# Kernel tuning notes

Measured on AMD Instinct MI355X. Metric: run time of the kernel, lower is better.

The kernel has to match this reference:

```python
import jax, jax.numpy as jnp
import numpy as np

N = 50000       # nodes
D_IN = 256      # in_channels
D_OUT = 256     # out_channels
E1 = 300000     # edges for TAGConv branch
E2 = 300000     # edges for attention branch


def setup_inputs() -> dict:
    key = jax.random.key(0)
    ks = jax.random.split(key, 8)
    s = 1.0 / np.sqrt(D_IN)  # torch Linear default init range
    u = lambda k: jax.random.uniform(k, (D_IN, D_OUT), jnp.float32, -s, s)
    return {
        "x": jax.random.normal(ks[0], (N, D_IN), jnp.float32),
        "edge_index": jax.random.randint(ks[1], (2, E1), 0, N),
        "edge_index_2": jax.random.randint(ks[2], (2, E2), 0, N),
        "W0": u(ks[3]),  # TAGConv hop-0 weight
        "W1": u(ks[4]),  # TAGConv hop-1 weight
        "Wq": u(ks[5]),  # attention query proj
        "Wk": u(ks[6]),  # attention key proj
        "Wv": u(ks[7]),  # attention value proj
    }


def reference(x, edge_index, edge_index_2, W0, W1, Wq, Wk, Wv):
    # --- TAGConv branch: K=1, normalize=False, bias=False ---
    src, dst = edge_index[0], edge_index[1]
    agg = jax.ops.segment_sum(x[src], dst, num_segments=N)   # A @ x, [N, D_IN]
    x1 = x @ W0 + agg @ W1                                   # [N, D_OUT]

    # --- Transformer_Block branch over edge_index_2, use_softmax=False ---
    q = x @ Wq
    k = x @ Wk
    v = x @ Wv
    s2, d2 = edge_index_2[0], edge_index_2[1]
    attn = jnp.einsum('ed,ed->e', q[d2], k[s2])              # per-edge raw score
    x2 = jax.ops.segment_sum(attn[:, None] * v[s2], d2, num_segments=N)

    return x1 - x2
```

## Files before the change

kernel.cpp:

```cpp
#include <hip/hip_runtime.h>

#define TD 256

typedef __attribute__((ext_vector_type(8))) short short8;
typedef __attribute__((ext_vector_type(8))) unsigned short ushort8;
typedef __attribute__((ext_vector_type(4))) float f32x4;

__device__ inline unsigned short f2bf(float f) {
  unsigned u = __float_as_uint(f);
  u = u + 0x7fffu + ((u >> 16) & 1u);
  return (unsigned short)(u >> 16);
}
__device__ inline float bf2f(unsigned short h) {
  return __uint_as_float(((unsigned)h) << 16);
}

__global__ __launch_bounds__(256) void prologue_kernel(
    const int* __restrict__ ei, int E1, const int* __restrict__ ei2, int E2,
    int* __restrict__ deg1, int* __restrict__ deg2,
    const float* __restrict__ x, unsigned short* __restrict__ xb, long total8,
    const float* __restrict__ Wq, const float* __restrict__ Wk,
    unsigned short* __restrict__ wqb, unsigned short* __restrict__ wkb,
    const float* __restrict__ W0, const float* __restrict__ W1,
    const float* __restrict__ Wv, unsigned short* __restrict__ wt,
    int nbH, int nbX) {
  int b = blockIdx.x;
  if (b < nbH) {
    int stride = nbH * 256;
    int Emax = max(E1, E2);
    for (int i = b * 256 + threadIdx.x; i < Emax; i += stride) {
      if (i < E1) atomicAdd(&deg1[ei[E1 + i]], 1);
      if (i < E2) atomicAdd(&deg2[ei2[E2 + i]], 1);
    }
  } else if (b < nbH + nbX) {
    long t = (long)(b - nbH) * 256 + threadIdx.x;
    if (t >= total8) return;
    const float4 f0 = *reinterpret_cast<const float4*>(x + t * 8);
    const float4 f1 = *reinterpret_cast<const float4*>(x + t * 8 + 4);
    ushort8 o;
    o[0] = f2bf(f0.x); o[1] = f2bf(f0.y); o[2] = f2bf(f0.z); o[3] = f2bf(f0.w);
    o[4] = f2bf(f1.x); o[5] = f2bf(f1.y); o[6] = f2bf(f1.z); o[7] = f2bf(f1.w);
    *reinterpret_cast<ushort8*>(xb + t * 8) = o;
  } else if (b < nbH + nbX + 64) {
    int t = (b - nbH - nbX) * 256 + threadIdx.x;
    const float* src = (t < 8192) ? Wq : Wk;
    unsigned short* dst = (t < 8192) ? wqb : wkb;
    int o = (t & 8191) * 8;
    ushort8 r;
#pragma unroll
    for (int j = 0; j < 8; j++) r[j] = f2bf(src[o + j]);
    *reinterpret_cast<ushort8*>(dst + o) = r;
  } else {
    int b2 = b - nbH - nbX - 64;
    int m = b2 >> 8;
    int n = b2 & 255;
    int k = threadIdx.x;
    const float* W = m == 0 ? W0 : m == 1 ? W1 : Wv;
    wt[m * 65536 + n * 256 + k] = f2bf(W[k * 256 + n]);
  }
}

__global__ __launch_bounds__(256) void scanA_gemmG_kernel(
    const int* __restrict__ deg1, const int* __restrict__ deg2, int N,
    int* __restrict__ bsum,
    const unsigned short* __restrict__ wqb, const unsigned short* __restrict__ wkb,
    unsigned short* __restrict__ gt) {
  if (blockIdx.x < 512) {
    int arr = blockIdx.x >> 8;
    int b = blockIdx.x & 255;
    const int* deg = arr ? deg2 : deg1;
    int i = b * 256 + threadIdx.x;
    int v = (i < N) ? deg[i] : 0;
#pragma unroll
    for (int m = 1; m < 64; m <<= 1) v += __shfl_xor(v, m, 64);
    __shared__ int wsum[4];
    if ((threadIdx.x & 63) == 0) wsum[threadIdx.x >> 6] = v;
    __syncthreads();
    if (threadIdx.x == 0)
      bsum[blockIdx.x] = wsum[0] + wsum[1] + wsum[2] + wsum[3];
    return;
  }
  const int t = (blockIdx.x - 512) * 4 + (threadIdx.x >> 6);
  const int l = threadIdx.x & 63;
  const int a0 = (t >> 2) * 64;
  const int b0 = (t & 3) * 64;
  const int lc = l & 15;
  const int lk = l >> 4;
  f32x4 acc[4][4] = {};
#pragma unroll
  for (int ks = 0; ks < 256; ks += 32) {
    const int ko = ks + lk * 8;
    short8 a[4], b[4];
#pragma unroll
    for (int m = 0; m < 4; m++)
      a[m] = *reinterpret_cast<const short8*>(wqb + (a0 + m * 16 + lc) * 256 + ko);
#pragma unroll
    for (int n = 0; n < 4; n++)
      b[n] = *reinterpret_cast<const short8*>(wkb + (b0 + n * 16 + lc) * 256 + ko);
#pragma unroll
    for (int m = 0; m < 4; m++)
#pragma unroll
      for (int n = 0; n < 4; n++)
        acc[m][n] =
            __builtin_amdgcn_mfma_f32_16x16x32_bf16(a[m], b[n], acc[m][n], 0, 0, 0);
  }
#pragma unroll
  for (int m = 0; m < 4; m++)
#pragma unroll
    for (int n = 0; n < 4; n++)
#pragma unroll
      for (int j = 0; j < 4; j++) {
        int a = a0 + m * 16 + lk * 4 + j;
        int b = b0 + n * 16 + lc;
        gt[b * 256 + a] = f2bf(acc[m][n][j]);
      }
}

__global__ __launch_bounds__(256) void scan_fill_kernel(
    const int* __restrict__ deg1, const int* __restrict__ deg2,
    const int* __restrict__ bsum, int N,
    int* __restrict__ off1, int* __restrict__ cur1,
    int* __restrict__ off2, int* __restrict__ cur2) {
  int arr = blockIdx.x >> 8;
  int b = blockIdx.x & 255;
  const int* deg = arr ? deg2 : deg1;
  int* off = arr ? off2 : off1;
  int* cur = arr ? cur2 : cur1;
  const int t = threadIdx.x;

  __shared__ int redp[4], redt[4];
  int sval = bsum[arr * 256 + t];
  int pv = (t < b) ? sval : 0;
  int tv = sval;
#pragma unroll
  for (int m = 1; m < 64; m <<= 1) {
    pv += __shfl_xor(pv, m, 64);
    tv += __shfl_xor(tv, m, 64);
  }
  if ((t & 63) == 0) { redp[t >> 6] = pv; redt[t >> 6] = tv; }
  __syncthreads();
  int prefix = redp[0] + redp[1] + redp[2] + redp[3];
  int total = redt[0] + redt[1] + redt[2] + redt[3];
  if (b == 255 && t == 0) off[N] = total;

  int i = b * 256 + t;
  __shared__ int sm[256];
  int v = (i < N) ? deg[i] : 0;
  sm[t] = v;
  __syncthreads();
  for (int d = 1; d < 256; d <<= 1) {
    int val = (t >= d) ? sm[t - d] : 0;
    __syncthreads();
    sm[t] += val;
    __syncthreads();
  }
  int e = sm[t] - v + prefix;
  if (i < N) {
    off[i] = e;
    cur[i] = e;
  }
}

__global__ __launch_bounds__(512) void fill_gemm0_kernel(
    const int* __restrict__ ei, int E1, const int* __restrict__ ei2, int E2,
    int* __restrict__ cur1, int* __restrict__ cur2,
    int* __restrict__ csr1, int* __restrict__ csr2,
    const unsigned short* __restrict__ xb, const unsigned short* __restrict__ gt,
    unsigned short* __restrict__ qb, int M, int FB) {
  __shared__ __align__(16) unsigned short sA[128 * 64];
  __shared__ __align__(16) unsigned short sB[256 * 64];

  if (blockIdx.x < FB) {
    int stride = FB * 512;
    int Emax = max(E1, E2);
    for (int i = blockIdx.x * 512 + threadIdx.x; i < Emax; i += stride) {
      if (i < E1) {
        int d = ei[E1 + i];
        int p = atomicAdd(&cur1[d], 1);
        csr1[p] = ei[i];
      }
      if (i < E2) {
        int d = ei2[E2 + i];
        int p = atomicAdd(&cur2[d], 1);
        csr2[p] = ei2[i];
      }
    }
    return;
  }

  const int m0 = (blockIdx.x - FB) * 128;
  const int tid = threadIdx.x;
  const int w = tid >> 6, l = tid & 63;
  const int lrow = l >> 3, lslot = l & 7;
  const int wr = w >> 2, wc = w & 3;

  f32x4 acc[4][4] = {};

  for (int k0 = 0; k0 < 256; k0 += 64) {
    const unsigned short* Ap = xb;
    const unsigned short* Bp = gt;
    int ks = k0;

#pragma unroll
    for (int i = 0; i < 2; i++) {
      int row = w * 16 + i * 8 + lrow;
      int gr = m0 + row;
      if (gr >= M) gr = M - 1;
      int g = lslot ^ lrow;
      const unsigned short* src = Ap + (size_t)gr * TD + ks + g * 8;
      unsigned short* dst = sA + (w * 16 + i * 8) * 64;
      __builtin_amdgcn_global_load_lds(
          (const __attribute__((address_space(1))) void*)src,
          (__attribute__((address_space(3))) void*)dst, 16, 0, 0);
    }
#pragma unroll
    for (int i = 0; i < 4; i++) {
      int row = w * 32 + i * 8 + lrow;
      int g = lslot ^ lrow;
      const unsigned short* src = Bp + (size_t)row * TD + ks + g * 8;
      unsigned short* dst = sB + (w * 32 + i * 8) * 64;
      __builtin_amdgcn_global_load_lds(
          (const __attribute__((address_space(1))) void*)src,
          (__attribute__((address_space(3))) void*)dst, 16, 0, 0);
    }
    __syncthreads();

#pragma unroll
    for (int kk = 0; kk < 2; kk++) {
      short8 a[4], b[4];
#pragma unroll
      for (int m = 0; m < 4; m++) {
        int row = wr * 64 + m * 16 + (l & 15);
        int slot = (kk * 4 + (l >> 4)) ^ (row & 7);
        a[m] = *reinterpret_cast<const short8*>(&sA[row * 64 + slot * 8]);
      }
#pragma unroll
      for (int n = 0; n < 4; n++) {
        int row = wc * 64 + n * 16 + (l & 15);
        int slot = (kk * 4 + (l >> 4)) ^ (row & 7);
        b[n] = *reinterpret_cast<const short8*>(&sB[row * 64 + slot * 8]);
      }
#pragma unroll
      for (int m = 0; m < 4; m++)
#pragma unroll
        for (int n = 0; n < 4; n++)
          acc[m][n] =
              __builtin_amdgcn_mfma_f32_16x16x32_bf16(a[m], b[n], acc[m][n], 0, 0, 0);
    }
    __syncthreads();
  }

#pragma unroll
  for (int m = 0; m < 4; m++)
#pragma unroll
    for (int n = 0; n < 4; n++)
#pragma unroll
      for (int j = 0; j < 4; j++) {
        int r = m0 + wr * 64 + m * 16 + (l >> 4) * 4 + j;
        if (r < M)
          qb[(size_t)r * TD + wc * 64 + n * 16 + (l & 15)] = f2bf(acc[m][n][j]);
      }
}

__global__ __launch_bounds__(256) void gather_fused_kernel(
    const unsigned short* __restrict__ xb, const unsigned short* __restrict__ qb,
    const int* __restrict__ off1, const int* __restrict__ csr1,
    const int* __restrict__ off2, const int* __restrict__ csr2,
    int N, unsigned short* __restrict__ aggb, unsigned short* __restrict__ tb) {
  int wid = blockIdx.x * 4 + (threadIdx.x >> 6);
  if (wid >= N) return;
  const int lane = threadIdx.x & 63;
  const int eh = lane >> 5;
  const int sl = lane & 31;

  {
    int beg = off1[wid], end = off1[wid + 1];
    float acc[8] = {};
    for (int j = beg; j < end; j += 4) {
      int e1 = end - 1;
      int j0 = j + eh, j1 = j + 2 + eh;
      int s0 = csr1[j0 < end ? j0 : e1];
      int s1 = csr1[j1 < end ? j1 : e1];
      float k0 = (j0 < end) ? 1.f : 0.f;
      float k1 = (j1 < end) ? 1.f : 0.f;
      ushort8 r0 = *reinterpret_cast<const ushort8*>(xb + (size_t)s0 * TD + sl * 8);
      ushort8 r1 = *reinterpret_cast<const ushort8*>(xb + (size_t)s1 * TD + sl * 8);
#pragma unroll
      for (int i = 0; i < 8; i++)
        acc[i] += k0 * bf2f(r0[i]) + k1 * bf2f(r1[i]);
    }
#pragma unroll
    for (int i = 0; i < 8; i++) acc[i] += __shfl_xor(acc[i], 32, 64);
    if (eh == 0) {
      ushort8 o;
#pragma unroll
      for (int i = 0; i < 8; i++) o[i] = f2bf(acc[i]);
      *reinterpret_cast<ushort8*>(aggb + (size_t)wid * TD + sl * 8) = o;
    }
  }

  {
    ushort8 qv = *reinterpret_cast<const ushort8*>(qb + (size_t)wid * TD + sl * 8);
    float q[8];
#pragma unroll
    for (int i = 0; i < 8; i++) q[i] = bf2f(qv[i]);
    int beg = off2[wid], end = off2[wid + 1];
    float t[8] = {};
    for (int j = beg; j < end; j += 4) {
      int e1 = end - 1;
      int j0 = j + eh, j1 = j + 2 + eh;
      int s0 = csr2[j0 < end ? j0 : e1];
      int s1 = csr2[j1 < end ? j1 : e1];
      float k0 = (j0 < end) ? 1.f : 0.f;
      float k1 = (j1 < end) ? 1.f : 0.f;
      ushort8 r0 = *reinterpret_cast<const ushort8*>(xb + (size_t)s0 * TD + sl * 8);
      ushort8 r1 = *reinterpret_cast<const ushort8*>(xb + (size_t)s1 * TD + sl * 8);
      float x0[8], x1[8];
      float p0 = 0.f, p1 = 0.f;
#pragma unroll
      for (int i = 0; i < 8; i++) {
        x0[i] = bf2f(r0[i]); x1[i] = bf2f(r1[i]);
        p0 += q[i] * x0[i];  p1 += q[i] * x1[i];
      }
#pragma unroll
      for (int m = 1; m < 32; m <<= 1) {
        p0 += __shfl_xor(p0, m, 64);
        p1 += __shfl_xor(p1, m, 64);
      }
      p0 *= k0; p1 *= k1;
#pragma unroll
      for (int i = 0; i < 8; i++) t[i] -= p0 * x0[i] + p1 * x1[i];
    }
#pragma unroll
    for (int i = 0; i < 8; i++) t[i] += __shfl_xor(t[i], 32, 64);
    if (eh == 0) {
      ushort8 o;
#pragma unroll
      for (int i = 0; i < 8; i++) o[i] = f2bf(t[i]);
      *reinterpret_cast<ushort8*>(tb + (size_t)wid * TD + sl * 8) = o;
    }
  }
}

__global__ __launch_bounds__(512) void gemm1_kernel(
    const unsigned short* __restrict__ xb, const unsigned short* __restrict__ aggb,
    const unsigned short* __restrict__ tb, const unsigned short* __restrict__ wt,
    float* __restrict__ out, int M) {
  __shared__ __align__(16) unsigned short sA[128 * 64];
  __shared__ __align__(16) unsigned short sB[256 * 64];

  const int m0 = blockIdx.x * 128;
  const int tid = threadIdx.x;
  const int w = tid >> 6, l = tid & 63;
  const int lrow = l >> 3, lslot = l & 7;
  const int wr = w >> 2, wc = w & 3;

  f32x4 acc[4][4] = {};

  for (int k0 = 0; k0 < 768; k0 += 64) {
    int seg = k0 >> 8;
    const unsigned short* Ap = seg == 0 ? xb : seg == 1 ? aggb : tb;
    const unsigned short* Bp = wt + seg * 65536;
    int ks = k0 & 255;

#pragma unroll
    for (int i = 0; i < 2; i++) {
      int row = w * 16 + i * 8 + lrow;
      int gr = m0 + row;
      if (gr >= M) gr = M - 1;
      int g = lslot ^ lrow;
      const unsigned short* src = Ap + (size_t)gr * TD + ks + g * 8;
      unsigned short* dst = sA + (w * 16 + i * 8) * 64;
      __builtin_amdgcn_global_load_lds(
          (const __attribute__((address_space(1))) void*)src,
          (__attribute__((address_space(3))) void*)dst, 16, 0, 0);
    }
#pragma unroll
    for (int i = 0; i < 4; i++) {
      int row = w * 32 + i * 8 + lrow;
      int g = lslot ^ lrow;
      const unsigned short* src = Bp + (size_t)row * TD + ks + g * 8;
      unsigned short* dst = sB + (w * 32 + i * 8) * 64;
      __builtin_amdgcn_global_load_lds(
          (const __attribute__((address_space(1))) void*)src,
          (__attribute__((address_space(3))) void*)dst, 16, 0, 0);
    }
    __syncthreads();

#pragma unroll
    for (int kk = 0; kk < 2; kk++) {
      short8 a[4], b[4];
#pragma unroll
      for (int m = 0; m < 4; m++) {
        int row = wr * 64 + m * 16 + (l & 15);
        int slot = (kk * 4 + (l >> 4)) ^ (row & 7);
        a[m] = *reinterpret_cast<const short8*>(&sA[row * 64 + slot * 8]);
      }
#pragma unroll
      for (int n = 0; n < 4; n++) {
        int row = wc * 64 + n * 16 + (l & 15);
        int slot = (kk * 4 + (l >> 4)) ^ (row & 7);
        b[n] = *reinterpret_cast<const short8*>(&sB[row * 64 + slot * 8]);
      }
#pragma unroll
      for (int m = 0; m < 4; m++)
#pragma unroll
        for (int n = 0; n < 4; n++)
          acc[m][n] =
              __builtin_amdgcn_mfma_f32_16x16x32_bf16(a[m], b[n], acc[m][n], 0, 0, 0);
    }
    __syncthreads();
  }

#pragma unroll
  for (int m = 0; m < 4; m++)
#pragma unroll
    for (int n = 0; n < 4; n++)
#pragma unroll
      for (int j = 0; j < 4; j++) {
        int r = m0 + wr * 64 + m * 16 + (l >> 4) * 4 + j;
        if (r < M)
          out[(size_t)r * TD + wc * 64 + n * 16 + (l & 15)] = acc[m][n][j];
      }
}

extern "C" void kernel_launch(void* const* d_in, const int* in_sizes, int n_in,
                              void* d_out, int out_size, void* d_ws,
                              size_t ws_size, hipStream_t stream) {
  const float* x  = (const float*)d_in[0];
  const int*   ei  = (const int*)d_in[1];
  const int*   ei2 = (const int*)d_in[2];
  const float* W0 = (const float*)d_in[3];
  const float* W1 = (const float*)d_in[4];
  const float* Wq = (const float*)d_in[5];
  const float* Wk = (const float*)d_in[6];
  const float* Wv = (const float*)d_in[7];

  const int N  = in_sizes[0] / TD;
  const int E1 = in_sizes[1] / 2;
  const int E2 = in_sizes[2] / 2;

  float* out = (float*)d_out;
  const size_t rowN = (size_t)N * TD;

  char* p = (char*)d_ws;
  unsigned short* xb   = (unsigned short*)p; p += rowN * 2;
  unsigned short* aggb = (unsigned short*)p; p += rowN * 2;
  unsigned short* qb   = (unsigned short*)p; p += rowN * 2;
  unsigned short* tb   = (unsigned short*)p; p += rowN * 2;
  unsigned short* wt   = (unsigned short*)p; p += 3 * 65536 * 2;
  unsigned short* gt   = (unsigned short*)p; p += 65536 * 2;
  unsigned short* wqb  = (unsigned short*)p; p += 65536 * 2;
  unsigned short* wkb  = (unsigned short*)p; p += 65536 * 2;
  int* off1 = (int*)p; p += (N + 1) * 4;
  int* cur1 = (int*)p; p += N * 4;
  int* off2 = (int*)p; p += (N + 1) * 4;
  int* cur2 = (int*)p; p += N * 4;
  int* csr1 = (int*)p; p += (size_t)E1 * 4;
  int* csr2 = (int*)p; p += (size_t)E2 * 4;
  int* deg1 = (int*)p; p += N * 4;
  int* deg2 = (int*)p; p += N * 4;
  int* bsum = (int*)p; p += 512 * 4;

  hipMemsetAsync(deg1, 0, (size_t)2 * N * sizeof(int), stream);

  long total8 = rowN / 8;
  int nbH = 512;
  int nbX = (int)((total8 + 255) / 256);
  prologue_kernel<<<nbH + nbX + 64 + 768, 256, 0, stream>>>(
      ei, E1, ei2, E2, deg1, deg2, x, xb, total8, Wq, Wk, wqb, wkb, W0, W1, Wv,
      wt, nbH, nbX);

  scanA_gemmG_kernel<<<516, 256, 0, stream>>>(deg1, deg2, N, bsum, wqb, wkb, gt);
  scan_fill_kernel<<<512, 256, 0, stream>>>(deg1, deg2, bsum, N, off1, cur1,
                                            off2, cur2);

  int gblk = (N + 127) / 128;
  int FB = 384;
  fill_gemm0_kernel<<<FB + gblk, 512, 0, stream>>>(
      ei, E1, ei2, E2, cur1, cur2, csr1, csr2, xb, gt, qb, N, FB);

  gather_fused_kernel<<<(N + 3) / 4, 256, 0, stream>>>(xb, qb, off1, csr1,
                                                       off2, csr2, N, aggb, tb);

  gemm1_kernel<<<gblk, 512, 0, stream>>>(xb, aggb, tb, wt, out, N);
}
```

Measured before the change: 178.2 us.

## Overlap x@W0 GEMM slice with edge gather in one fused launch

Moves the x@W0 part of the final GEMM into the gather kernel as extra blocks, so the compute-bound MFMA work can run alongside the memory-bound gather. The final GEMM then covers only the agg and t segments and adds its result into out. The gather blocks grow to 512 threads (8 waves) and take on the GEMM's shared-memory footprint, which may lower occupancy for the gather. The final GEMM also adds a read-modify-write of the fp32 output.

Result: slower. 227.4 us (+27.6%).

```diff
diff --git a/kernel.cpp b/kernel.cpp
--- a/kernel.cpp
+++ b/kernel.cpp
@@ -262,12 +262,92 @@
       }
 }
 
-__global__ __launch_bounds__(256) void gather_fused_kernel(
+__global__ __launch_bounds__(512) void gather_xw0_kernel(
     const unsigned short* __restrict__ xb, const unsigned short* __restrict__ qb,
     const int* __restrict__ off1, const int* __restrict__ csr1,
     const int* __restrict__ off2, const int* __restrict__ csr2,
-    int N, unsigned short* __restrict__ aggb, unsigned short* __restrict__ tb) {
-  int wid = blockIdx.x * 4 + (threadIdx.x >> 6);
+    int N, unsigned short* __restrict__ aggb, unsigned short* __restrict__ tb,
+    const unsigned short* __restrict__ wt, float* __restrict__ out, int gblk) {
+  __shared__ __align__(16) unsigned short sA[128 * 64];
+  __shared__ __align__(16) unsigned short sB[256 * 64];
+
+  if (blockIdx.x < gblk) {
+    const int m0 = blockIdx.x * 128;
+    const int tid = threadIdx.x;
+    const int w = tid >> 6, l = tid & 63;
+    const int lrow = l >> 3, lslot = l & 7;
+    const int wr = w >> 2, wc = w & 3;
+
+    f32x4 acc[4][4] = {};
+
+    for (int k0 = 0; k0 < 256; k0 += 64) {
+      const unsigned short* Ap = xb;
+      const unsigned short* Bp = wt;
+      int ks = k0;
+
+#pragma unroll
+      for (int i = 0; i < 2; i++) {
+        int row = w * 16 + i * 8 + lrow;
+        int gr = m0 + row;
+        if (gr >= N) gr = N - 1;
+        int g = lslot ^ lrow;
+        const unsigned short* src = Ap + (size_t)gr * TD + ks + g * 8;
+        unsigned short* dst = sA + (w * 16 + i * 8) * 64;
+        __builtin_amdgcn_global_load_lds(
+            (const __attribute__((address_space(1))) void*)src,
+            (__attribute__((address_space(3))) void*)dst, 16, 0, 0);
+      }
+#pragma unroll
+      for (int i = 0; i < 4; i++) {
+        int row = w * 32 + i * 8 + lrow;
+        int g = lslot ^ lrow;
+        const unsigned short* src = Bp + (size_t)row * TD + ks + g * 8;
+        unsigned short* dst = sB + (w * 32 + i * 8) * 64;
+        __builtin_amdgcn_global_load_lds(
+            (const __attribute__((address_space(1))) void*)src,
+            (__attribute__((address_space(3))) void*)dst, 16, 0, 0);
+      }
+      __syncthreads();
+
+#pragma unroll
+      for (int kk = 0; kk < 2; kk++) {
+        short8 a[4], b[4];
+#pragma unroll
+        for (int m = 0; m < 4; m++) {
+          int row = wr * 64 + m * 16 + (l & 15);
+          int slot = (kk * 4 + (l >> 4)) ^ (row & 7);
+          a[m] = *reinterpret_cast<const short8*>(&sA[row * 64 + slot * 8]);
+        }
+#pragma unroll
+        for (int n = 0; n < 4; n++) {
+          int row = wc * 64 + n * 16 + (l & 15);
+          int slot = (kk * 4 + (l >> 4)) ^ (row & 7);
+          b[n] = *reinterpret_cast<const short8*>(&sB[row * 64 + slot * 8]);
+        }
+#pragma unroll
+        for (int m = 0; m < 4; m++)
+#pragma unroll
+          for (int n = 0; n < 4; n++)
+            acc[m][n] =
+                __builtin_amdgcn_mfma_f32_16x16x32_bf16(a[m], b[n], acc[m][n], 0, 0, 0);
+      }
+      __syncthreads();
+    }
+
+#pragma unroll
+    for (int m = 0; m < 4; m++)
+#pragma unroll
+      for (int n = 0; n < 4; n++)
+#pragma unroll
+        for (int j = 0; j < 4; j++) {
+          int r = m0 + wr * 64 + m * 16 + (l >> 4) * 4 + j;
+          if (r < N)
+            out[(size_t)r * TD + wc * 64 + n * 16 + (l & 15)] = acc[m][n][j];
+        }
+    return;
+  }
+
+  int wid = (blockIdx.x - gblk) * 8 + (threadIdx.x >> 6);
   if (wid >= N) return;
   const int lane = threadIdx.x & 63;
   const int eh = lane >> 5;
@@ -343,9 +423,8 @@
 }
 
 __global__ __launch_bounds__(512) void gemm1_kernel(
-    const unsigned short* __restrict__ xb, const unsigned short* __restrict__ aggb,
-    const unsigned short* __restrict__ tb, const unsigned short* __restrict__ wt,
-    float* __restrict__ out, int M) {
+    const unsigned short* __restrict__ aggb, const unsigned short* __restrict__ tb,
+    const unsigned short* __restrict__ wt, float* __restrict__ out, int M) {
   __shared__ __align__(16) unsigned short sA[128 * 64];
   __shared__ __align__(16) unsigned short sB[256 * 64];
 
@@ -357,10 +436,10 @@
 
   f32x4 acc[4][4] = {};
 
-  for (int k0 = 0; k0 < 768; k0 += 64) {
+  for (int k0 = 0; k0 < 512; k0 += 64) {
     int seg = k0 >> 8;
-    const unsigned short* Ap = seg == 0 ? xb : seg == 1 ? aggb : tb;
-    const unsigned short* Bp = wt + seg * 65536;
+    const unsigned short* Ap = seg == 0 ? aggb : tb;
+    const unsigned short* Bp = wt + (seg + 1) * 65536;
     int ks = k0 & 255;
 
 #pragma unroll
@@ -419,8 +498,10 @@
 #pragma unroll
       for (int j = 0; j < 4; j++) {
         int r = m0 + wr * 64 + m * 16 + (l >> 4) * 4 + j;
-        if (r < M)
-          out[(size_t)r * TD + wc * 64 + n * 16 + (l & 15)] = acc[m][n][j];
+        if (r < M) {
+          size_t idx = (size_t)r * TD + wc * 64 + n * 16 + (l & 15);
+          out[idx] = out[idx] + acc[m][n][j];
+        }
       }
 }
 
@@ -480,8 +561,9 @@
   fill_gemm0_kernel<<<FB + gblk, 512, 0, stream>>>(
       ei, E1, ei2, E2, cur1, cur2, csr1, csr2, xb, gt, qb, N, FB);
 
-  gather_fused_kernel<<<(N + 3) / 4, 256, 0, stream>>>(xb, qb, off1, csr1,
-                                                       off2, csr2, N, aggb, tb);
-
-  gemm1_kernel<<<gblk, 512, 0, stream>>>(xb, aggb, tb, wt, out, N);
-}
+  int GB = (N + 7) / 8;
+  gather_xw0_kernel<<<gblk + GB, 512, 0, stream>>>(
+      xb, qb, off1, csr1, off2, csr2, N, aggb, tb, wt, out, gblk);
+
+  gemm1_kernel<<<gblk, 512, 0, stream>>>(aggb, tb, wt, out, N);
+}
```

## Move x@W0 GEMM segment into earlier fill_gemm0 kernel and accumulate later

Applied to the files above, without the earlier changes.

The x@W0 part of the final GEMM now runs as extra blocks in the fill/gemm0 kernel. It writes fp32 partial results to out, and the final GEMM only processes the agg and t segments before adding into out. The aim is to shorten the critical-path final GEMM and overlap that work with the CSR fill and Q GEMM. In exchange, out is written and then read back as fp32, which adds global memory traffic, and the earlier kernel gets more blocks.

Measured after the change: 197.8 us. +11.0%, slower.

```diff
diff --git a/kernel.cpp b/kernel.cpp
--- a/kernel.cpp
+++ b/kernel.cpp
@@ -161,12 +161,73 @@
   }
 }
 
+__device__ __forceinline__ void gemm_tile_k256(
+    const unsigned short* __restrict__ Ap, const unsigned short* __restrict__ Bp,
+    int m0, int M, unsigned short* sA, unsigned short* sB, f32x4 (&acc)[4][4]) {
+  const int tid = threadIdx.x;
+  const int w = tid >> 6, l = tid & 63;
+  const int lrow = l >> 3, lslot = l & 7;
+  const int wr = w >> 2, wc = w & 3;
+
+  for (int k0 = 0; k0 < 256; k0 += 64) {
+#pragma unroll
+    for (int i = 0; i < 2; i++) {
+      int row = w * 16 + i * 8 + lrow;
+      int gr = m0 + row;
+      if (gr >= M) gr = M - 1;
+      int g = lslot ^ lrow;
+      const unsigned short* src = Ap + (size_t)gr * TD + k0 + g * 8;
+      unsigned short* dst = sA + (w * 16 + i * 8) * 64;
+      __builtin_amdgcn_global_load_lds(
+          (const __attribute__((address_space(1))) void*)src,
+          (__attribute__((address_space(3))) void*)dst, 16, 0, 0);
+    }
+#pragma unroll
+    for (int i = 0; i < 4; i++) {
+      int row = w * 32 + i * 8 + lrow;
+      int g = lslot ^ lrow;
+      const unsigned short* src = Bp + (size_t)row * TD + k0 + g * 8;
+      unsigned short* dst = sB + (w * 32 + i * 8) * 64;
+      __builtin_amdgcn_global_load_lds(
+          (const __attribute__((address_space(1))) void*)src,
+          (__attribute__((address_space(3))) void*)dst, 16, 0, 0);
+    }
+    __syncthreads();
+
+#pragma unroll
+    for (int kk = 0; kk < 2; kk++) {
+      short8 a[4], b[4];
+#pragma unroll
+      for (int m = 0; m < 4; m++) {
+        int row = wr * 64 + m * 16 + (l & 15);
+        int slot = (kk * 4 + (l >> 4)) ^ (row & 7);
+        a[m] = *reinterpret_cast<const short8*>(&sA[row * 64 + slot * 8]);
+      }
+#pragma unroll
+      for (int n = 0; n < 4; n++) {
+        int row = wc * 64 + n * 16 + (l & 15);
+        int slot = (kk * 4 + (l >> 4)) ^ (row & 7);
+        b[n] = *reinterpret_cast<const short8*>(&sB[row * 64 + slot * 8]);
+      }
+#pragma unroll
+      for (int m = 0; m < 4; m++)
+#pragma unroll
+        for (int n = 0; n < 4; n++)
+          acc[m][n] =
+              __builtin_amdgcn_mfma_f32_16x16x32_bf16(a[m], b[n], acc[m][n], 0, 0, 0);
+    }
+    __syncthreads();
+  }
+}
+
 __global__ __launch_bounds__(512) void fill_gemm0_kernel(
     const int* __restrict__ ei, int E1, const int* __restrict__ ei2, int E2,
     int* __restrict__ cur1, int* __restrict__ cur2,
     int* __restrict__ csr1, int* __restrict__ csr2,
     const unsigned short* __restrict__ xb, const unsigned short* __restrict__ gt,
-    unsigned short* __restrict__ qb, int M, int FB) {
+    const unsigned short* __restrict__ wt,
+    unsigned short* __restrict__ qb, float* __restrict__ out, int M, int FB,
+    int gblk) {
   __shared__ __align__(16) unsigned short sA[128 * 64];
   __shared__ __align__(16) unsigned short sB[256 * 64];
 
@@ -188,78 +249,38 @@
     return;
   }
 
-  const int m0 = (blockIdx.x - FB) * 128;
-  const int tid = threadIdx.x;
-  const int w = tid >> 6, l = tid & 63;
-  const int lrow = l >> 3, lslot = l & 7;
+  const int gb = blockIdx.x - FB;
+  const bool isQ = gb < gblk;
+  const int m0 = (isQ ? gb : gb - gblk) * 128;
+  f32x4 acc[4][4] = {};
+  gemm_tile_k256(xb, isQ ? gt : wt, m0, M, sA, sB, acc);
+
+  const int l = threadIdx.x & 63;
+  const int w = threadIdx.x >> 6;
   const int wr = w >> 2, wc = w & 3;
-
-  f32x4 acc[4][4] = {};
-
-  for (int k0 = 0; k0 < 256; k0 += 64) {
-    const unsigned short* Ap = xb;
-    const unsigned short* Bp = gt;
-    int ks = k0;
-
-#pragma unroll
-    for (int i = 0; i < 2; i++) {
-      int row = w * 16 + i * 8 + lrow;
-      int gr = m0 + row;
-      if (gr >= M) gr = M - 1;
-      int g = lslot ^ lrow;
-      const unsigned short* src = Ap + (size_t)gr * TD + ks + g * 8;
-      unsigned short* dst = sA + (w * 16 + i * 8) * 64;
-      __builtin_amdgcn_global_load_lds(
-          (const __attribute__((address_space(1))) void*)src,
-          (__attribute__((address_space(3))) void*)dst, 16, 0, 0);
-    }
-#pragma unroll
-    for (int i = 0; i < 4; i++) {
-      int row = w * 32 + i * 8 + lrow;
-      int g = lslot ^ lrow;
-      const unsigned short* src = Bp + (size_t)row * TD + ks + g * 8;
-      unsigned short* dst = sB + (w * 32 + i * 8) * 64;
-      __builtin_amdgcn_global_load_lds(
-          (const __attribute__((address_space(1))) void*)src,
-          (__attribute__((address_space(3))) void*)dst, 16, 0, 0);
-    }
-    __syncthreads();
-
-#pragma unroll
-    for (int kk = 0; kk < 2; kk++) {
-      short8 a[4], b[4];
-#pragma unroll
-      for (int m = 0; m < 4; m++) {
-        int row = wr * 64 + m * 16 + (l & 15);
-        int slot = (kk * 4 + (l >> 4)) ^ (row & 7);
-        a[m] = *reinterpret_cast<const short8*>(&sA[row * 64 + slot * 8]);
-      }
-#pragma unroll
-      for (int n = 0; n < 4; n++) {
-        int row = wc * 64 + n * 16 + (l & 15);
-        int slot = (kk * 4 + (l >> 4)) ^ (row & 7);
-        b[n] = *reinterpret_cast<const short8*>(&sB[row * 64 + slot * 8]);
-      }
-#pragma unroll
-      for (int m = 0; m < 4; m++)
-#pragma unroll
-        for (int n = 0; n < 4; n++)
-          acc[m][n] =
-              __builtin_amdgcn_mfma_f32_16x16x32_bf16(a[m], b[n], acc[m][n], 0, 0, 0);
-    }
-    __syncthreads();
-  }
-
-#pragma unroll
-  for (int m = 0; m < 4; m++)
-#pragma unroll
-    for (int n = 0; n < 4; n++)
-#pragma unroll
-      for (int j = 0; j < 4; j++) {
-        int r = m0 + wr * 64 + m * 16 + (l >> 4) * 4 + j;
-        if (r < M)
-          qb[(size_t)r * TD + wc * 64 + n * 16 + (l & 15)] = f2bf(acc[m][n][j]);
-      }
+  if (isQ) {
+#pragma unroll
+    for (int m = 0; m < 4; m++)
+#pragma unroll
+      for (int n = 0; n < 4; n++)
+#pragma unroll
+        for (int j = 0; j < 4; j++) {
+          int r = m0 + wr * 64 + m * 16 + (l >> 4) * 4 + j;
+          if (r < M)
+            qb[(size_t)r * TD + wc * 64 + n * 16 + (l & 15)] = f2bf(acc[m][n][j]);
+        }
+  } else {
+#pragma unroll
+    for (int m = 0; m < 4; m++)
+#pragma unroll
+      for (int n = 0; n < 4; n++)
+#pragma unroll
+        for (int j = 0; j < 4; j++) {
+          int r = m0 + wr * 64 + m * 16 + (l >> 4) * 4 + j;
+          if (r < M)
+            out[(size_t)r * TD + wc * 64 + n * 16 + (l & 15)] = acc[m][n][j];
+        }
+  }
 }
 
 __global__ __launch_bounds__(256) void gather_fused_kernel(
@@ -343,9 +364,8 @@
 }
 
 __global__ __launch_bounds__(512) void gemm1_kernel(
-    const unsigned short* __restrict__ xb, const unsigned short* __restrict__ aggb,
-    const unsigned short* __restrict__ tb, const unsigned short* __restrict__ wt,
-    float* __restrict__ out, int M) {
+    const unsigned short* __restrict__ aggb, const unsigned short* __restrict__ tb,
+    const unsigned short* __restrict__ wt, float* __restrict__ out, int M) {
   __shared__ __align__(16) unsigned short sA[128 * 64];
   __shared__ __align__(16) unsigned short sB[256 * 64];
 
@@ -357,10 +377,10 @@
 
   f32x4 acc[4][4] = {};
 
-  for (int k0 = 0; k0 < 768; k0 += 64) {
+  for (int k0 = 0; k0 < 512; k0 += 64) {
     int seg = k0 >> 8;
-    const unsigned short* Ap = seg == 0 ? xb : seg == 1 ? aggb : tb;
-    const unsigned short* Bp = wt + seg * 65536;
+    const unsigned short* Ap = seg == 0 ? aggb : tb;
+    const unsigned short* Bp = wt + (seg + 1) * 65536;
     int ks = k0 & 255;
 
 #pragma unroll
@@ -419,8 +439,10 @@
 #pragma unroll
       for (int j = 0; j < 4; j++) {
         int r = m0 + wr * 64 + m * 16 + (l >> 4) * 4 + j;
-        if (r < M)
-          out[(size_t)r * TD + wc * 64 + n * 16 + (l & 15)] = acc[m][n][j];
+        if (r < M) {
+          size_t idx = (size_t)r * TD + wc * 64 + n * 16 + (l & 15);
+          out[idx] = out[idx] + acc[m][n][j];
+        }
       }
 }
 
@@ -477,11 +499,11 @@
 
   int gblk = (N + 127) / 128;
   int FB = 384;
-  fill_gemm0_kernel<<<FB + gblk, 512, 0, stream>>>(
-      ei, E1, ei2, E2, cur1, cur2, csr1, csr2, xb, gt, qb, N, FB);
+  fill_gemm0_kernel<<<FB + 2 * gblk, 512, 0, stream>>>(
+      ei, E1, ei2, E2, cur1, cur2, csr1, csr2, xb, gt, wt, qb, out, N, FB, gblk);
 
   gather_fused_kernel<<<(N + 3) / 4, 256, 0, stream>>>(xb, qb, off1, csr1,
                                                        off2, csr2, N, aggb, tb);
 
-  gemm1_kernel<<<gblk, 512, 0, stream>>>(xb, aggb, tb, wt, out, N);
-}
+  gemm1_kernel<<<gblk, 512, 0, stream>>>(aggb, tb, wt, out, N);
+}
```
